# Optimization experiments

Measured on AMD Instinct MI355X. Metric: run time of the kernel, lower is better.

Reference implementation:

```python
import jax, jax.numpy as jnp
import numpy as np

D_MODEL = 1024
N_HEADS = 16
D_HEAD = D_MODEL // N_HEADS


def setup_inputs() -> dict:
    key = jax.random.key(0)
    k1, k2, k3 = jax.random.split(key, 3)
    B, T = 2, 2048
    x = jax.random.normal(k1, (B, T, D_MODEL), dtype=jnp.float32)
    key_padding_mask = jnp.zeros((B, T), dtype=bool)  # True = padded key
    # nn.Linear weights: [out_features, in_features], bias=False
    W_qkv = jax.random.normal(k2, (3 * D_MODEL, D_MODEL), dtype=jnp.float32) * (D_MODEL ** -0.5)
    W_proj = jax.random.normal(k3, (D_MODEL, D_MODEL), dtype=jnp.float32) * (D_MODEL ** -0.5)
    return {"x": x, "key_padding_mask": key_padding_mask, "W_qkv": W_qkv, "W_proj": W_proj}


def reference(x, key_padding_mask, W_qkv, W_proj):
    B, T, D = x.shape
    H, Dh = N_HEADS, D_HEAD
    scale = Dh ** -0.5
    # qkv: [B,T,3D] -> [3,B,H,T,Dh]
    qkv = (x @ W_qkv.T).reshape(B, T, 3, H, Dh).transpose(2, 0, 3, 1, 4)
    q, k, v = qkv[0], qkv[1], qkv[2]
    # attention scores [B,H,T,T]
    attn = jnp.einsum("bhqd,bhkd->bhqk", q, k) * scale
    attn = jnp.where(key_padding_mask[:, None, None, :], -jnp.inf, attn)
    attn = jax.nn.softmax(attn, axis=-1)  # dropout in eval mode = identity
    out = jnp.einsum("bhqk,bhkd->bhqd", attn, v)
    out = out.transpose(0, 2, 1, 3).reshape(B, T, D)
    return out @ W_proj.T
```

## Files before the change

### kernel.cpp

```cpp
#include <hip/hip_runtime.h>
#include <hip/hip_bf16.h>

typedef unsigned short u16;
typedef unsigned int u32;
typedef __bf16 bf16x8 __attribute__((ext_vector_type(8)));
typedef float f32x4 __attribute__((ext_vector_type(4)));
typedef float f32x16 __attribute__((ext_vector_type(16)));

#define DMODEL 1024
#define NH 16
#define DH 64
#define BB 2
#define TT 2048
#define MM 4096
#define NQKV 3072
#define KVB 128

#define QSCALE 0.18033688011112042f

static __device__ __forceinline__ u16 f2bf(float f) {
  u32 u = __float_as_uint(f);
  u = (u + 0x7FFFu + ((u >> 16) & 1u)) >> 16;
  return (u16)u;
}

static __device__ __forceinline__ u32 pk2bf(float a, float b) {
  u16 ua = __builtin_bit_cast(u16, (__bf16)a);
  u16 ub = __builtin_bit_cast(u16, (__bf16)b);
  return (u32)ua | ((u32)ub << 16);
}

static __device__ __forceinline__ float fexp2(float x) {
#if __has_builtin(__builtin_amdgcn_exp2f)
  return __builtin_amdgcn_exp2f(x);
#else
  float r; asm("v_exp_f32 %0, %1" : "=v"(r) : "v"(x)); return r;
#endif
}

static __device__ __forceinline__ float max3f(float a, float b, float c) {
  return fmaxf(fmaxf(a, b), c);
}

static __device__ __forceinline__ float maxv16(const f32x16& v) {
  float t0 = max3f(v[0], v[1], v[2]);
  float t1 = max3f(v[3], v[4], v[5]);
  float t2 = max3f(v[6], v[7], v[8]);
  float t3 = max3f(v[9], v[10], v[11]);
  float t4 = max3f(v[12], v[13], v[14]);
  return fmaxf(max3f(t0, t1, t2), max3f(t3, t4, v[15]));
}

static __device__ __forceinline__ void gload16(const u16* g, u16* l) {
  __builtin_amdgcn_global_load_lds(
      (const __attribute__((address_space(1))) void*)g,
      (__attribute__((address_space(3))) void*)l, 16, 0, 0);
}

#define N4X  (MM * DMODEL / 4)
#define N4W  (NQKV * DMODEL / 4)
#define N4P  (DMODEL * DMODEL / 4)
__global__ __launch_bounds__(256) void cvt_all(const float* __restrict__ x,
                                               const float* __restrict__ wqkv,
                                               const float* __restrict__ wproj,
                                               u16* __restrict__ dst) {
  int i = blockIdx.x * 256 + threadIdx.x;
  const float* src;
  int j = i;
  if (i < N4X) {
    src = x;
  } else if (i < N4X + N4W) {
    src = wqkv; j = i - N4X;
  } else {
    src = wproj; j = i - (N4X + N4W);
  }
  float4 v = reinterpret_cast<const float4*>(src)[j];
  ushort4 o;
  o.x = f2bf(v.x); o.y = f2bf(v.y); o.z = f2bf(v.z); o.w = f2bf(v.w);
  reinterpret_cast<ushort4*>(dst)[i] = o;
}

static __device__ __forceinline__ void gemm_stage(
    const u16* __restrict__ A, const u16* __restrict__ B, u16* As, u16* Bs,
    int r0, int o0, int r1, int o1, int c0, int c1, int kcol) {
  gload16(A + (size_t)r0 * DMODEL + kcol + o0, As + c0 * 8);
  gload16(A + (size_t)r1 * DMODEL + kcol + o1, As + c1 * 8);
  gload16(B + (size_t)r0 * DMODEL + kcol + o0, Bs + c0 * 8);
  gload16(B + (size_t)r1 * DMODEL + kcol + o1, Bs + c1 * 8);
}

static __device__ __forceinline__ void gemm128_mainloop(
    const u16* __restrict__ Abase, const u16* __restrict__ Bbase,
    u16* As, u16* Bs, f32x4 (&acc)[4][4]) {
  const int tid = threadIdx.x;
  const int lane = tid & 63;
  const int w = tid >> 6;
  const int rowg = lane >> 4, col = lane & 15;
  const int wm = w >> 1, wn = w & 1;
  const int c0 = tid, c1 = tid + 256;
  const int r0 = c0 >> 2, o0 = (c0 & 3) * 8;
  const int r1 = c1 >> 2, o1 = (c1 & 3) * 8;

  gemm_stage(Abase, Bbase, As, Bs, r0, o0, r1, o1, c0, c1, 0);
  asm volatile("s_waitcnt vmcnt(0)" ::: "memory");
  __builtin_amdgcn_s_barrier();

  int sel = 0;
  for (int kt = 0; kt < DMODEL / 32; ++kt) {
    const int kn = ((kt + 1) & (DMODEL / 32 - 1)) * 32;
    const int ns = sel ^ 1;
    gemm_stage(Abase, Bbase, As + ns * 4096, Bs + ns * 4096, r0, o0, r1, o1, c0, c1, kn);
    const u16* as = As + sel * 4096;
    const u16* bs = Bs + sel * 4096;
    bf16x8 af[4], bfr[4];
#pragma unroll
    for (int i = 0; i < 4; ++i)
      af[i] = *reinterpret_cast<const bf16x8*>(as + (wm * 64 + i * 16 + col) * 32 + rowg * 8);
#pragma unroll
    for (int j = 0; j < 4; ++j)
      bfr[j] = *reinterpret_cast<const bf16x8*>(bs + (wn * 64 + j * 16 + col) * 32 + rowg * 8);
#pragma unroll
    for (int i = 0; i < 4; ++i)
#pragma unroll
      for (int j = 0; j < 4; ++j)
        acc[i][j] = __builtin_amdgcn_mfma_f32_16x16x32_bf16(af[i], bfr[j], acc[i][j], 0, 0, 0);
    asm volatile("s_waitcnt vmcnt(0)" ::: "memory");
    __builtin_amdgcn_s_barrier();
    sel = ns;
  }
}

__global__ __launch_bounds__(256, 3) void qkv_gemm(
    const u16* __restrict__ xb, const u16* __restrict__ wb,
    u16* __restrict__ qb, u16* __restrict__ kb, u16* __restrict__ vtb) {
  __shared__ u16 As[2 * 128 * 32];
  __shared__ u16 Bs[2 * 128 * 32];
  f32x4 acc[4][4];
#pragma unroll
  for (int i = 0; i < 4; ++i)
#pragma unroll
    for (int j = 0; j < 4; ++j) acc[i][j] = (f32x4){0.f, 0.f, 0.f, 0.f};
  gemm128_mainloop(xb + (size_t)blockIdx.y * 128 * DMODEL,
                   wb + (size_t)blockIdx.x * 128 * DMODEL, As, Bs, acc);
  const int lane = threadIdx.x & 63, w = threadIdx.x >> 6;
  const int rowg = lane >> 4, col = lane & 15, wm = w >> 1, wn = w & 1;
#pragma unroll
  for (int i = 0; i < 4; ++i) {
#pragma unroll
    for (int j = 0; j < 4; ++j) {
#pragma unroll
      for (int r = 0; r < 4; ++r) {
        int m = blockIdx.y * 128 + wm * 64 + i * 16 + rowg * 4 + r;
        int n = blockIdx.x * 128 + wn * 64 + j * 16 + col;
        int b = m >> 11, t = m & (TT - 1);
        int s = n >> 10, h = (n >> 6) & 15, d = n & 63;
        int bh = b * NH + h;
        float v = acc[i][j][r];
        if (s == 0)      qb[((size_t)bh * TT + t) * DH + d] = f2bf(v * QSCALE);
        else if (s == 1) kb[((size_t)bh * TT + t) * DH + d] = f2bf(v);
        else             vtb[((size_t)bh * DH + d) * TT + t] = f2bf(v);
      }
    }
  }
}

__global__ __launch_bounds__(256, 3) void proj_gemm(
    const u16* __restrict__ ab, const u16* __restrict__ wb, float* __restrict__ out) {
  __shared__ u16 As[2 * 128 * 32];
  __shared__ u16 Bs[2 * 128 * 32];
  f32x4 acc[4][4];
#pragma unroll
  for (int i = 0; i < 4; ++i)
#pragma unroll
    for (int j = 0; j < 4; ++j) acc[i][j] = (f32x4){0.f, 0.f, 0.f, 0.f};
  gemm128_mainloop(ab + (size_t)blockIdx.y * 128 * DMODEL,
                   wb + (size_t)blockIdx.x * 128 * DMODEL, As, Bs, acc);
  const int lane = threadIdx.x & 63, w = threadIdx.x >> 6;
  const int rowg = lane >> 4, col = lane & 15, wm = w >> 1, wn = w & 1;
#pragma unroll
  for (int i = 0; i < 4; ++i) {
#pragma unroll
    for (int j = 0; j < 4; ++j) {
#pragma unroll
      for (int r = 0; r < 4; ++r) {
        int m = blockIdx.y * 128 + wm * 64 + i * 16 + rowg * 4 + r;
        int n = blockIdx.x * 128 + wn * 64 + j * 16 + col;
        out[(size_t)m * DMODEL + n] = acc[i][j][r];
      }
    }
  }
}

static __device__ __forceinline__ void attn_stage(
    const u16* __restrict__ kbase, const u16* __restrict__ vbase,
    int kt, u16* KsSel, u16* VsSel, int tid) {
#pragma unroll
  for (int p = 0; p < 4; ++p) {
    int c = p * 256 + tid;
    int row = c >> 3;
    int bI = (c & 7) * 16;
    gload16(kbase + kt * (KVB * DH) + row * DH + ((bI ^ ((row & 7) << 4)) >> 1), KsSel + c * 8);
  }
#pragma unroll
  for (int p = 0; p < 4; ++p) {
    int c = p * 256 + tid;
    int d = c >> 4;
    int bI = (c & 15) * 16;
    gload16(vbase + (size_t)d * TT + kt * KVB + ((bI ^ ((d & 7) << 4)) >> 1), VsSel + c * 8);
  }
}

__global__ __launch_bounds__(256, 2) void attn_kernel(
    const u16* __restrict__ qb, const u16* __restrict__ kb,
    const u16* __restrict__ vtb, const unsigned char* __restrict__ mask,
    u16* __restrict__ ob) {
  __shared__ u16 SM[2][2][KVB * DH];
  __shared__ unsigned char maskb[TT];
  __shared__ u32 mflag;

  const int tid = threadIdx.x;
  const int lane = tid & 63, w = tid >> 6;
  const int col = lane & 31, h = lane >> 5;
  const int qt = blockIdx.x, bh = blockIdx.y;
  const int b = bh >> 4;

  if (tid == 0) mflag = 0;
  __syncthreads();

  {
    const u32* mg = reinterpret_cast<const u32*>(mask + (size_t)b * TT);
    u32 m0 = mg[tid * 2], m1 = mg[tid * 2 + 1];
    *reinterpret_cast<u32*>(maskb + tid * 8) = m0;
    *reinterpret_cast<u32*>(maskb + tid * 8 + 4) = m1;
    if (m0 | m1) atomicOr(&mflag, 1u << (tid >> 4));
  }

  const int qrow0 = qt * 128 + w * 32;
  const u16* qptr = qb + ((size_t)bh * TT + qrow0) * DH;
  bf16x8 aq[4];
#pragma unroll
  for (int dstep = 0; dstep < 4; ++dstep)
    aq[dstep] = *reinterpret_cast<const bf16x8*>(qptr + col * DH + dstep * 16 + h * 8);

  f32x16 acc[2];
#pragma unroll
  for (int df = 0; df < 2; ++df)
#pragma unroll
    for (int r = 0; r < 16; ++r) acc[df][r] = 0.f;
  float m_run = -1e30f, l_run = 0.f;

  const u16* kbase = kb + (size_t)bh * TT * DH;
  const u16* vbase = vtb + (size_t)bh * DH * TT;

  attn_stage(kbase, vbase, 0, SM[0][0], SM[0][1], tid);
  __syncthreads();
  const u32 fm = mflag;

  int cur = 0;
  for (int t = 0; t < TT / KVB; ++t) {
    const int tn = (t + 1) & (TT / KVB - 1);
    attn_stage(kbase, vbase, tn, SM[cur ^ 1][0], SM[cur ^ 1][1], tid);

    const u16* ks = SM[cur][0];
    const u16* vs = SM[cur][1];

    f32x16 sc[4];
#pragma unroll
    for (int kf = 0; kf < 4; ++kf)
#pragma unroll
      for (int r = 0; r < 16; ++r) sc[kf][r] = 0.f;
#pragma unroll
    for (int dstep = 0; dstep < 4; ++dstep) {
      bf16x8 ak[4];
#pragma unroll
      for (int kf = 0; kf < 4; ++kf) {
        int row = kf * 32 + col;
        ak[kf] = *reinterpret_cast<const bf16x8*>(
            ks + row * DH + (((dstep * 32 + h * 16) ^ ((row & 7) << 4)) >> 1));
      }
#pragma unroll
      for (int kf = 0; kf < 4; ++kf)
        sc[kf] = __builtin_amdgcn_mfma_f32_32x32x16_bf16(ak[kf], aq[dstep], sc[kf], 0, 0, 0);
    }

    if (fm & (1u << t)) {
#pragma unroll
      for (int kf = 0; kf < 4; ++kf)
#pragma unroll
        for (int r = 0; r < 16; ++r) {
          int key = kf * 32 + (r & 3) + 8 * (r >> 2) + 4 * h;
          sc[kf][r] += maskb[t * KVB + key] ? -1e30f : 0.f;
        }
    }

    u32 P2[4][8];
    {
      float mk0 = maxv16(sc[0]), mk1 = maxv16(sc[1]);
      float mk2 = maxv16(sc[2]), mk3 = maxv16(sc[3]);
      float mx = fmaxf(fmaxf(mk0, mk1), fmaxf(mk2, mk3));
      mx = fmaxf(mx, __shfl_xor(mx, 32, 64));
      if (__any(mx > m_run + 8.0f)) {
        float mn = fmaxf(m_run, mx);
        float corr = fexp2(m_run - mn);
        m_run = mn;
        l_run *= corr;
#pragma unroll
        for (int df = 0; df < 2; ++df)
#pragma unroll
          for (int r = 0; r < 16; ++r) acc[df][r] *= corr;
      }
      const float mc = m_run;
      float rs = 0.f;
#pragma unroll
      for (int kf = 0; kf < 4; ++kf) {
#pragma unroll
        for (int i = 0; i < 8; ++i) {
          float p0 = fexp2(sc[kf][2 * i] - mc);
          float p1 = fexp2(sc[kf][2 * i + 1] - mc);
          rs += p0 + p1;
          P2[kf][i] = pk2bf(p0, p1);
        }
      }
      rs += __shfl_xor(rs, 32, 64);
      l_run += rs;
    }

    __builtin_amdgcn_s_setprio(1);
#pragma unroll
    for (int ksl = 0; ksl < 8; ++ksl) {
      const int kf = ksl >> 1;
      const int i0 = (ksl & 1) * 4;
      u32 w0 = P2[kf][i0],     w2 = P2[kf][i0 + 2];
      u32 w1 = P2[kf][i0 + 1], w3 = P2[kf][i0 + 3];
      asm("v_permlane32_swap_b32 %0, %1" : "+v"(w0), "+v"(w2));
      asm("v_permlane32_swap_b32 %0, %1" : "+v"(w1), "+v"(w3));
      u32 bpw[4] = {w0, w1, w2, w3};
      bf16x8 bp = __builtin_bit_cast(bf16x8, *reinterpret_cast<uint4*>(bpw));
#pragma unroll
      for (int df = 0; df < 2; ++df) {
        int row = df * 32 + col;
        bf16x8 av = *reinterpret_cast<const bf16x8*>(
            vs + row * KVB + (((ksl * 32 + h * 16) ^ ((row & 7) << 4)) >> 1));
        acc[df] = __builtin_amdgcn_mfma_f32_32x32x16_bf16(av, bp, acc[df], 0, 0, 0);
      }
    }
    __builtin_amdgcn_s_setprio(0);

    asm volatile("s_waitcnt vmcnt(0)" ::: "memory");
    __builtin_amdgcn_s_barrier();
    cur ^= 1;
  }

  u16* Ol = &SM[0][0][0];
  {
    float inv = 1.f / l_run;
    const int q = w * 32 + col;
    const int swzq = (q ^ (q >> 3)) & 7;
#pragma unroll
    for (int df = 0; df < 2; ++df) {
#pragma unroll
      for (int a = 0; a < 4; ++a) {
        uint2 pk;
        pk.x = pk2bf(acc[df][4 * a] * inv, acc[df][4 * a + 1] * inv);
        pk.y = pk2bf(acc[df][4 * a + 2] * inv, acc[df][4 * a + 3] * inv);
        int d2 = df * 64 + a * 16 + h * 8;
        int byte = q * 128 + (d2 ^ (swzq << 4));
        *reinterpret_cast<uint2*>(reinterpret_cast<char*>(Ol) + byte) = pk;
      }
    }
  }
  __syncthreads();
  {
    const int hh = bh & 15;
#pragma unroll
    for (int p = 0; p < 4; ++p) {
      int idx = p * 256 + tid;
      int q = idx >> 3, ch = idx & 7;
      int swzq = (q ^ (q >> 3)) & 7;
      uint4 v = *reinterpret_cast<const uint4*>(
          reinterpret_cast<const char*>(Ol) + q * 128 + ((ch * 16) ^ (swzq << 4)));
      size_t row = (size_t)(b * TT + qt * 128 + q);
      *reinterpret_cast<uint4*>(ob + row * DMODEL + hh * DH + ch * 8) = v;
    }
  }
}

extern "C" void kernel_launch(void* const* d_in, const int* in_sizes, int n_in,
                              void* d_out, int out_size, void* d_ws, size_t ws_size,
                              hipStream_t stream) {
  const float* x = (const float*)d_in[0];
  const unsigned char* mask = (const unsigned char*)d_in[1];
  const float* wqkv = (const float*)d_in[2];
  const float* wproj = (const float*)d_in[3];
  float* out = (float*)d_out;

  u16* xb     = (u16*)d_ws;
  u16* wqkvb  = xb    + (size_t)MM * DMODEL;
  u16* wprojb = wqkvb + (size_t)NQKV * DMODEL;
  u16* qb     = wprojb + (size_t)DMODEL * DMODEL;
  u16* kb     = qb + (size_t)MM * DMODEL;
  u16* vtb    = kb + (size_t)MM * DMODEL;
  u16* ob     = vtb + (size_t)MM * DMODEL;

  cvt_all<<<(N4X + N4W + N4P) / 256, 256, 0, stream>>>(x, wqkv, wproj, xb);
  qkv_gemm<<<dim3(NQKV / 128, MM / 128), 256, 0, stream>>>(xb, wqkvb, qb, kb, vtb);
  attn_kernel<<<dim3(TT / 128, BB * NH), 256, 0, stream>>>(qb, kb, vtb, mask, ob);
  proj_gemm<<<dim3(DMODEL / 128, MM / 128), 256, 0, stream>>>(ob, wprojb, out);
}
```

Baseline: 133.8 us.

## Software-pipeline attention: overlap previous tile's PV MFMAs with current softmax exp

Restructures the flash-attention inner loop so that the P·V MFMAs for the previous KV tile run interleaved with the exponentials and bf16 packing of the current tile. The previous tile's probabilities, V fragments (preloaded into registers) and rescale factor are carried across iterations, and a drain step after the loop finishes the last tile. The aim is to hide softmax VALU latency behind matrix-core work. In exchange it holds many more live registers (16 V fragments plus 32 packed P words), which may lower occupancy or cause spills.

```diff
diff --git a/kernel.cpp b/kernel.cpp
--- a/kernel.cpp
+++ b/kernel.cpp
@@ -249,12 +249,42 @@
     for (int r = 0; r < 16; ++r) acc[df][r] = 0.f;
   float m_run = -1e30f, l_run = 0.f;
 
+  bf16x8 vprev[16];
+  u32 P2_prev[4][8];
+  float corr_prev = 1.f, rs_prev = 0.f;
+  bool resc_prev = false;
+  {
+    bf16x8 z = {};
+#pragma unroll
+    for (int i = 0; i < 16; ++i) vprev[i] = z;
+#pragma unroll
+    for (int kf = 0; kf < 4; ++kf)
+#pragma unroll
+      for (int i = 0; i < 8; ++i) P2_prev[kf][i] = 0;
+  }
+
   const u16* kbase = kb + (size_t)bh * TT * DH;
   const u16* vbase = vtb + (size_t)bh * DH * TT;
 
   attn_stage(kbase, vbase, 0, SM[0][0], SM[0][1], tid);
   __syncthreads();
   const u32 fm = mflag;
+
+#define PVG(KSL)                                                                      \
+  {                                                                                   \
+    const int kf_ = (KSL) >> 1;                                                       \
+    const int i0_ = ((KSL) & 1) * 4;                                                  \
+    u32 w0 = P2_prev[kf_][i0_],     w2 = P2_prev[kf_][i0_ + 2];                       \
+    u32 w1 = P2_prev[kf_][i0_ + 1], w3 = P2_prev[kf_][i0_ + 3];                       \
+    asm("v_permlane32_swap_b32 %0, %1" : "+v"(w0), "+v"(w2));                         \
+    asm("v_permlane32_swap_b32 %0, %1" : "+v"(w1), "+v"(w3));                         \
+    u32 bpw[4] = {w0, w1, w2, w3};                                                    \
+    bf16x8 bp = __builtin_bit_cast(bf16x8, *reinterpret_cast<uint4*>(bpw));           \
+    acc[0] = __builtin_amdgcn_mfma_f32_32x32x16_bf16(vprev[(KSL) * 2 + 0], bp,        \
+                                                     acc[0], 0, 0, 0);                \
+    acc[1] = __builtin_amdgcn_mfma_f32_32x32x16_bf16(vprev[(KSL) * 2 + 1], bp,        \
+                                                     acc[1], 0, 0, 0);                \
+  }
 
   int cur = 0;
   for (int t = 0; t < TT / KVB; ++t) {
@@ -293,63 +323,81 @@
         }
     }
 
-    u32 P2[4][8];
+    float mx;
     {
       float mk0 = maxv16(sc[0]), mk1 = maxv16(sc[1]);
       float mk2 = maxv16(sc[2]), mk3 = maxv16(sc[3]);
-      float mx = fmaxf(fmaxf(mk0, mk1), fmaxf(mk2, mk3));
+      mx = fmaxf(fmaxf(mk0, mk1), fmaxf(mk2, mk3));
       mx = fmaxf(mx, __shfl_xor(mx, 32, 64));
-      if (__any(mx > m_run + 8.0f)) {
-        float mn = fmaxf(m_run, mx);
-        float corr = fexp2(m_run - mn);
-        m_run = mn;
-        l_run *= corr;
-#pragma unroll
-        for (int df = 0; df < 2; ++df)
-#pragma unroll
-          for (int r = 0; r < 16; ++r) acc[df][r] *= corr;
-      }
-      const float mc = m_run;
-      float rs = 0.f;
-#pragma unroll
-      for (int kf = 0; kf < 4; ++kf) {
-#pragma unroll
-        for (int i = 0; i < 8; ++i) {
-          float p0 = fexp2(sc[kf][2 * i] - mc);
-          float p1 = fexp2(sc[kf][2 * i + 1] - mc);
-          rs += p0 + p1;
-          P2[kf][i] = pk2bf(p0, p1);
-        }
-      }
-      rs += __shfl_xor(rs, 32, 64);
-      l_run += rs;
-    }
-
+    }
+
+    if (resc_prev) {
+      l_run *= corr_prev;
+#pragma unroll
+      for (int df = 0; df < 2; ++df)
+#pragma unroll
+        for (int r = 0; r < 16; ++r) acc[df][r] *= corr_prev;
+    }
+    l_run += rs_prev;
+
+    bool resc = __any(mx > m_run + 8.0f);
+    float corr = 1.f;
+    if (resc) {
+      float mn = fmaxf(m_run, mx);
+      corr = fexp2(m_run - mn);
+      m_run = mn;
+    }
+    const float mc = m_run;
+
+    float rs = 0.f;
+    u32 P2c[4][8];
     __builtin_amdgcn_s_setprio(1);
 #pragma unroll
-    for (int ksl = 0; ksl < 8; ++ksl) {
-      const int kf = ksl >> 1;
-      const int i0 = (ksl & 1) * 4;
-      u32 w0 = P2[kf][i0],     w2 = P2[kf][i0 + 2];
-      u32 w1 = P2[kf][i0 + 1], w3 = P2[kf][i0 + 3];
-      asm("v_permlane32_swap_b32 %0, %1" : "+v"(w0), "+v"(w2));
-      asm("v_permlane32_swap_b32 %0, %1" : "+v"(w1), "+v"(w3));
-      u32 bpw[4] = {w0, w1, w2, w3};
-      bf16x8 bp = __builtin_bit_cast(bf16x8, *reinterpret_cast<uint4*>(bpw));
+    for (int g = 0; g < 4; ++g) {
+      PVG(2 * g);
+      PVG(2 * g + 1);
+#pragma unroll
+      for (int i = 0; i < 8; ++i) {
+        float p0 = fexp2(sc[g][2 * i] - mc);
+        float p1 = fexp2(sc[g][2 * i + 1] - mc);
+        rs += p0 + p1;
+        P2c[g][i] = pk2bf(p0, p1);
+      }
+    }
+    __builtin_amdgcn_s_setprio(0);
+    rs += __shfl_xor(rs, 32, 64);
+
+    resc_prev = resc; corr_prev = corr; rs_prev = rs;
+#pragma unroll
+    for (int kf = 0; kf < 4; ++kf)
+#pragma unroll
+      for (int i = 0; i < 8; ++i) P2_prev[kf][i] = P2c[kf][i];
+
+#pragma unroll
+    for (int ksl = 0; ksl < 8; ++ksl)
 #pragma unroll
       for (int df = 0; df < 2; ++df) {
         int row = df * 32 + col;
-        bf16x8 av = *reinterpret_cast<const bf16x8*>(
+        vprev[ksl * 2 + df] = *reinterpret_cast<const bf16x8*>(
             vs + row * KVB + (((ksl * 32 + h * 16) ^ ((row & 7) << 4)) >> 1));
-        acc[df] = __builtin_amdgcn_mfma_f32_32x32x16_bf16(av, bp, acc[df], 0, 0, 0);
-      }
-    }
-    __builtin_amdgcn_s_setprio(0);
-
-    asm volatile("s_waitcnt vmcnt(0)" ::: "memory");
+      }
+
+    asm volatile("s_waitcnt vmcnt(0) lgkmcnt(0)" ::: "memory");
     __builtin_amdgcn_s_barrier();
     cur ^= 1;
   }
+
+  if (resc_prev) {
+    l_run *= corr_prev;
+#pragma unroll
+    for (int df = 0; df < 2; ++df)
+#pragma unroll
+      for (int r = 0; r < 16; ++r) acc[df][r] *= corr_prev;
+  }
+  l_run += rs_prev;
+#pragma unroll
+  for (int ksl = 0; ksl < 8; ++ksl) PVG(ksl);
+#undef PVG
 
   u16* Ol = &SM[0][0][0];
   {
```

New measurement: 152.1 us. 1.14x slower.
